# Performance work log

Measured on AMD Instinct MI355X. Metric: run time of the kernel, lower is better.

Reference implementation:

```python
import jax, jax.numpy as jnp
import numpy as np

OUT = (4, 4, 4)       # output_size
SCALE = 1.0           # spatial_scale


def _axis_masks(start, length, n_bins, dim):
    """PyTorch AdaptiveMaxPool bin membership along one axis.

    bin i covers global indices [start + floor(i*L/O), start + ceil((i+1)*L/O)).
    Returns bool mask of shape [N, n_bins, dim].
    """
    i = jnp.arange(n_bins)
    bs = start[:, None] + (i[None, :] * length[:, None]) // n_bins
    be = start[:, None] - ((-(i[None, :] + 1) * length[:, None]) // n_bins)  # ceil div
    p = jnp.arange(dim)
    return (p[None, None, :] >= bs[:, :, None]) & (p[None, None, :] < be[:, :, None])


def _roi_pool_3d(x, rois):
    feat = x[0]                     # [C, X, Y, Z]
    C, X, Y, Z = feat.shape
    # rois: [1, N, 7] = (batch_idx, x0, y0, z0, x1, y1, z1); scale + round as in torch code
    r = jnp.round(rois[0, :, 1:].astype(jnp.float32) * SCALE).astype(jnp.int32)  # [N, 6]
    starts = r[:, :3]               # [N, 3]
    lens = r[:, 3:] + 1 - starts    # inclusive ends -> lengths, >= 1
    O1, O2, O3 = OUT
    mx = _axis_masks(starts[:, 0], lens[:, 0], O1, X)   # [N, O1, X]
    my = _axis_masks(starts[:, 1], lens[:, 1], O2, Y)   # [N, O2, Y]
    mz = _axis_masks(starts[:, 2], lens[:, 2], O3, Z)   # [N, O3, Z]
    neg = jnp.finfo(feat.dtype).min
    # separable max-reductions: z, then y, then x (loops are over the tiny fixed bin counts)
    t = jnp.stack([jnp.max(jnp.where(mz[:, k][:, None, None, None, :], feat[None], neg), axis=-1)
                   for k in range(O3)], axis=-1)                      # [N, C, X, Y, O3]
    t = jnp.stack([jnp.max(jnp.where(my[:, j][:, None, None, :, None], t, neg), axis=3)
                   for j in range(O2)], axis=3)                       # [N, C, X, O2, O3]
    t = jnp.stack([jnp.max(jnp.where(mx[:, i][:, None, :, None, None], t, neg), axis=2)
                   for i in range(O1)], axis=2)                       # [N, C, O1, O2, O3]
    return t


def setup_inputs() -> dict:
    key = jax.random.key(0)
    C, D, N = 64, 48, 16
    x = jax.random.normal(key, (1, C, D, D, D), dtype=jnp.float32)
    rng = np.random.default_rng(0)
    lens = rng.integers(8, 25, size=(N, 3))                       # roi extents in [8, 24]
    starts = np.array([rng.integers(0, D - L + 1) for L in lens.reshape(-1)]).reshape(N, 3)
    ends = starts + lens - 1                                      # inclusive ends, < D
    rois = np.concatenate([np.zeros((N, 1), np.int32),
                           starts.astype(np.int32),
                           ends.astype(np.int32)], axis=1)        # [N, 7]
    return {"input": x, "rois": jnp.asarray(rois[None], dtype=jnp.int32)}


def reference(input, rois):
    return _roi_pool_3d(input, rois)   # [N, C, 4, 4, 4]
```

## Files before the change

### kernel.cpp

```cpp
#include <hip/hip_runtime.h>
#include <float.h>

#define NC 64
#define DIM 48
#define NROI 16
#define NOUT (NROI * NC * 4 * 4 * 4)

__global__ __launch_bounds__(256) void roipool3d_kernel(
    const float* __restrict__ feat,
    const int*   __restrict__ rois,
    float*       __restrict__ out)
{
    int idx = blockIdx.x * 256 + threadIdx.x;
    if (idx >= NOUT) return;

    int k = idx & 3;
    int j = (idx >> 2) & 3;
    int i = (idx >> 4) & 3;
    int c = (idx >> 6) & (NC - 1);
    int n = idx >> 12;

    const int* r = rois + n * 7;
    int sx = r[1], sy = r[2], sz = r[3];
    int lx = r[4] + 1 - sx;
    int ly = r[5] + 1 - sy;
    int lz = r[6] + 1 - sz;

    int bx0 = sx + (i * lx) >> 2;
    bx0 = sx + ((i * lx) >> 2);
    int bx1 = sx + (((i + 1) * lx + 3) >> 2);
    int by0 = sy + ((j * ly) >> 2);
    int by1 = sy + (((j + 1) * ly + 3) >> 2);
    int bz0 = sz + ((k * lz) >> 2);
    int bz1 = sz + (((k + 1) * lz + 3) >> 2);

    const float* base = feat + (size_t)c * (DIM * DIM * DIM);

    float m = -FLT_MAX;
    for (int x = bx0; x < bx1; ++x) {
        for (int y = by0; y < by1; ++y) {
            const float* row = base + x * (DIM * DIM) + y * DIM;
            int z = bz0;
            for (; z + 3 < bz1; z += 4) {
                float a0 = row[z];
                float a1 = row[z + 1];
                float a2 = row[z + 2];
                float a3 = row[z + 3];
                m = fmaxf(m, fmaxf(fmaxf(a0, a1), fmaxf(a2, a3)));
            }
            for (; z < bz1; ++z) m = fmaxf(m, row[z]);
        }
    }
    out[idx] = m;
}

extern "C" void kernel_launch(void* const* d_in, const int* in_sizes, int n_in,
                              void* d_out, int out_size, void* d_ws, size_t ws_size,
                              hipStream_t stream) {
    const float* feat = (const float*)d_in[0];
    const int*   rois = (const int*)d_in[1];
    float*       out  = (float*)d_out;

    dim3 grid((NOUT + 255) / 256);
    dim3 block(256);
    roipool3d_kernel<<<grid, block, 0, stream>>>(feat, rois, out);
}
```

Baseline: 91.37 us.

## Split each bin's rows across four lanes and reduce with shuffles

Each block now handles one (roi, channel) pair, and four threads cooperate on each output bin. The bin's x-y rows are distributed across the four lanes and combined with xor shuffles. This gives four times as many threads and shortens each thread's serial loop. The cost is per-row div/mod index math, shuffle overhead, and only one in four lanes writing output.

```diff
diff --git a/kernel.cpp b/kernel.cpp
--- a/kernel.cpp
+++ b/kernel.cpp
@@ -4,21 +4,21 @@
 #define NC 64
 #define DIM 48
 #define NROI 16
-#define NOUT (NROI * NC * 4 * 4 * 4)
 
 __global__ __launch_bounds__(256) void roipool3d_kernel(
     const float* __restrict__ feat,
     const int*   __restrict__ rois,
     float*       __restrict__ out)
 {
-    int idx = blockIdx.x * 256 + threadIdx.x;
-    if (idx >= NOUT) return;
+    int t = threadIdx.x;
+    int bin = t >> 2;
+    int p   = t & 3;
+    int c = blockIdx.x & (NC - 1);
+    int n = blockIdx.x >> 6;
 
-    int k = idx & 3;
-    int j = (idx >> 2) & 3;
-    int i = (idx >> 4) & 3;
-    int c = (idx >> 6) & (NC - 1);
-    int n = idx >> 12;
+    int k = bin & 3;
+    int j = (bin >> 2) & 3;
+    int i = bin >> 4;
 
     const int* r = rois + n * 7;
     int sx = r[1], sy = r[2], sz = r[3];
@@ -26,32 +26,37 @@
     int ly = r[5] + 1 - sy;
     int lz = r[6] + 1 - sz;
 
-    int bx0 = sx + (i * lx) >> 2;
-    bx0 = sx + ((i * lx) >> 2);
+    int bx0 = sx + ((i * lx) >> 2);
     int bx1 = sx + (((i + 1) * lx + 3) >> 2);
     int by0 = sy + ((j * ly) >> 2);
     int by1 = sy + (((j + 1) * ly + 3) >> 2);
     int bz0 = sz + ((k * lz) >> 2);
     int bz1 = sz + (((k + 1) * lz + 3) >> 2);
 
+    int nx = bx1 - bx0;
+    int ny = by1 - by0;
+    int nrows = nx * ny;
+
     const float* base = feat + (size_t)c * (DIM * DIM * DIM);
 
-    float m = -FLT_MAX;
-    for (int x = bx0; x < bx1; ++x) {
-        for (int y = by0; y < by1; ++y) {
-            const float* row = base + x * (DIM * DIM) + y * DIM;
-            int z = bz0;
-            for (; z + 3 < bz1; z += 4) {
-                float a0 = row[z];
-                float a1 = row[z + 1];
-                float a2 = row[z + 2];
-                float a3 = row[z + 3];
-                m = fmaxf(m, fmaxf(fmaxf(a0, a1), fmaxf(a2, a3)));
-            }
-            for (; z < bz1; ++z) m = fmaxf(m, row[z]);
+    float m0 = -FLT_MAX, m1 = -FLT_MAX;
+    for (int rr = p; rr < nrows; rr += 4) {
+        int x = bx0 + rr / ny;
+        int y = by0 + rr % ny;
+        const float* row = base + x * (DIM * DIM) + y * DIM;
+        int z = bz0;
+        for (; z + 1 < bz1; z += 2) {
+            m0 = fmaxf(m0, row[z]);
+            m1 = fmaxf(m1, row[z + 1]);
         }
+        if (z < bz1) m0 = fmaxf(m0, row[z]);
     }
-    out[idx] = m;
+    float m = fmaxf(m0, m1);
+
+    m = fmaxf(m, __shfl_xor(m, 1));
+    m = fmaxf(m, __shfl_xor(m, 2));
+
+    if (p == 0) out[(blockIdx.x << 6) + bin] = m;
 }
 
 extern "C" void kernel_launch(void* const* d_in, const int* in_sizes, int n_in,
@@ -61,7 +66,5 @@
     const int*   rois = (const int*)d_in[1];
     float*       out  = (float*)d_out;
 
-    dim3 grid((NOUT + 255) / 256);
-    dim3 block(256);
-    roipool3d_kernel<<<grid, block, 0, stream>>>(feat, rois, out);
+    roipool3d_kernel<<<dim3(NROI * NC), dim3(256), 0, stream>>>(feat, rois, out);
 }
```

After: 75.63 us. 17.2% less time.
